# Kernel tuning notes

Measured on AMD Instinct MI355X. Metric: run time of the kernel, lower is better.

The kernel has to match this reference:

```python
import jax, jax.numpy as jnp
import numpy as np

EMB = 1024
E = 8        # num_experts
TOPK = 2
HID = 2048   # expert_dim

def setup_inputs() -> dict:
    key = jax.random.key(0)
    ks = jax.random.split(key, 10)
    s = lambda fan_in: 1.0 / np.sqrt(fan_in)
    x  = jax.random.normal(ks[0], (2, 2048, EMB), dtype=jnp.float32)
    Wr = jax.random.normal(ks[1], (EMB, E), dtype=jnp.float32) * s(EMB)
    br = jnp.zeros((E,), dtype=jnp.float32)
    # stacked expert weights, stored (in, out) so y = x @ W + b
    W1 = jax.random.normal(ks[2], (E, EMB, HID), dtype=jnp.float32) * s(EMB)
    b1 = jax.random.normal(ks[3], (E, HID), dtype=jnp.float32) * 0.01
    Wg = jax.random.normal(ks[4], (E, HID, HID), dtype=jnp.float32) * s(HID)
    bg = jax.random.normal(ks[5], (E, HID), dtype=jnp.float32) * 0.01
    W2 = jax.random.normal(ks[6], (E, HID, EMB), dtype=jnp.float32) * s(HID)
    b2 = jax.random.normal(ks[7], (E, EMB), dtype=jnp.float32) * 0.01
    return {"x": x, "Wr": Wr, "br": br, "W1": W1, "b1": b1,
            "Wg": Wg, "bg": bg, "W2": W2, "b2": b2}

def reference(x, Wr, br, W1, b1, Wg, bg, W2, b2):
    B, S, D = x.shape
    xt = x.reshape(B * S, D)                                  # [T, D]
    logits = xt @ Wr + br                                     # [T, E]
    probs = jax.nn.softmax(logits, axis=-1)
    topk_p, topk_i = jax.lax.top_k(probs, TOPK)               # [T, K]
    # dense gate matrix (top-k probs, NOT renormalized, as in source)
    gates = jnp.sum(jax.nn.one_hot(topk_i, E, dtype=xt.dtype) * topk_p[..., None], axis=1)  # [T, E]
    # expert MLP: layer1 (no act) -> relu(linear) -> layer2, for all experts
    h = jnp.einsum('td,edh->teh', xt, W1) + b1                # [T, E, HID]
    h = jax.nn.relu(jnp.einsum('teh,ehg->teg', h, Wg) + bg)   # [T, E, HID]
    y = jnp.einsum('teh,ehd->ted', h, W2) + b2                # [T, E, D]
    out = jnp.einsum('te,ted->td', gates, y)                  # weighted combine
    return out.reshape(B, S, D)
```

## Files before the change

### kernel.cpp

```cpp
#include <hip/hip_runtime.h>
#include <hip/hip_bf16.h>
#include <stdint.h>

#define NTOK 4096
#define EMBD 1024
#define NEXP 8
#define HIDD 2048
#define NPAIR (NTOK * 2)

typedef __attribute__((ext_vector_type(8))) __bf16 bf16x8;
typedef __attribute__((ext_vector_type(4))) float f32x4;

union V16 { uint4 u; bf16x8 b; };

__device__ __forceinline__ uint16_t f2bf(float f) {
    uint32_t u = __float_as_uint(f);
    return (uint16_t)((u + 0x7FFFu + ((u >> 16) & 1u)) >> 16);
}
__device__ __forceinline__ float bf2f(uint16_t u) {
    return __uint_as_float(((uint32_t)u) << 16);
}
__device__ __forceinline__ void gl_lds16(const uint16_t* g, uint16_t* l) {
    __builtin_amdgcn_global_load_lds(
        (const __attribute__((address_space(1))) void*)g,
        (__attribute__((address_space(3))) void*)l, 16, 0, 0);
}

#define W1_TILES 4096
#define WG_TILES 8192
#define W2_TILES 4096
__global__ __launch_bounds__(256) void transcast3_kernel(
    const float* __restrict__ W1, const float* __restrict__ Wg,
    const float* __restrict__ W2, uint16_t* __restrict__ W1t,
    uint16_t* __restrict__ Wgt, uint16_t* __restrict__ W2t) {
    int id = blockIdx.x;
    const float* src; uint16_t* dst; int K, N;
    if (id < W1_TILES) { src = W1; dst = W1t; K = EMBD; N = HIDD; }
    else if (id < W1_TILES + WG_TILES) { id -= W1_TILES; src = Wg; dst = Wgt; K = HIDD; N = HIDD; }
    else { id -= W1_TILES + WG_TILES; src = W2; dst = W2t; K = HIDD; N = EMBD; }
    int tn = N >> 6, tk = K >> 6;
    int per_e = tn * tk;
    int e = id / per_e, r = id % per_e;
    int n0 = (r % tn) * 64, k0 = (r / tn) * 64;

    __shared__ uint16_t tile[64][68];
    const float* S = src + ((size_t)e * K + k0) * N + n0;
    uint16_t* D = dst + ((size_t)e * N + n0) * K + k0;
    int t = threadIdx.x;
    int rn = (t & 15) * 4, rk = t >> 4;
#pragma unroll
    for (int p = 0; p < 4; p++) {
        int k = rk + p * 16;
        float4 v = *(const float4*)(S + (size_t)k * N + rn);
        ushort4 o;
        o.x = f2bf(v.x); o.y = f2bf(v.y); o.z = f2bf(v.z); o.w = f2bf(v.w);
        *(ushort4*)&tile[k][rn] = o;
    }
    __syncthreads();
    int wn = t >> 3, wk = (t & 7) * 8;
#pragma unroll
    for (int p = 0; p < 2; p++) {
        int n = wn + p * 32;
        uint32_t w0 = (uint32_t)tile[wk + 0][n] | ((uint32_t)tile[wk + 1][n] << 16);
        uint32_t w1 = (uint32_t)tile[wk + 2][n] | ((uint32_t)tile[wk + 3][n] << 16);
        uint32_t w2 = (uint32_t)tile[wk + 4][n] | ((uint32_t)tile[wk + 5][n] << 16);
        uint32_t w3 = (uint32_t)tile[wk + 6][n] | ((uint32_t)tile[wk + 7][n] << 16);
        uint4 pk = {w0, w1, w2, w3};
        *(uint4*)(D + (size_t)n * K + wk) = pk;
    }
}

__global__ __launch_bounds__(64) void router_kernel(const float* __restrict__ x,
                                                    const float* __restrict__ Wr,
                                                    const float* __restrict__ br,
                                                    uint16_t* __restrict__ xb,
                                                    int* __restrict__ counts,
                                                    int* __restrict__ pair_e,
                                                    float* __restrict__ pair_p) {
    int tok = blockIdx.x;
    int lane = threadIdx.x;
    const float* xr = x + (size_t)tok * EMBD;
    uint16_t* xbr = xb + (size_t)tok * EMBD;
    float acc[NEXP];
#pragma unroll
    for (int e = 0; e < NEXP; e++) acc[e] = 0.f;
    for (int d = lane; d < EMBD; d += 64) {
        float xv = xr[d];
        xbr[d] = f2bf(xv);
#pragma unroll
        for (int e = 0; e < NEXP; e++) acc[e] += xv * Wr[d * NEXP + e];
    }
#pragma unroll
    for (int e = 0; e < NEXP; e++) {
#pragma unroll
        for (int off = 32; off > 0; off >>= 1)
            acc[e] += __shfl_down(acc[e], off, 64);
    }
    if (lane == 0) {
        float lg[NEXP];
#pragma unroll
        for (int e = 0; e < NEXP; e++) lg[e] = acc[e] + br[e];
        int e0 = 0;
#pragma unroll
        for (int e = 1; e < NEXP; e++) if (lg[e] > lg[e0]) e0 = e;
        int e1 = (e0 == 0) ? 1 : 0;
#pragma unroll
        for (int e = 0; e < NEXP; e++) if (e != e0 && lg[e] > lg[e1]) e1 = e;
        float mx = lg[0];
#pragma unroll
        for (int e = 1; e < NEXP; e++) mx = fmaxf(mx, lg[e]);
        float s = 0.f, p[NEXP];
#pragma unroll
        for (int e = 0; e < NEXP; e++) { p[e] = __expf(lg[e] - mx); s += p[e]; }
        float inv = 1.f / s;
        pair_e[tok * 2 + 0] = e0; pair_p[tok * 2 + 0] = p[e0] * inv;
        pair_e[tok * 2 + 1] = e1; pair_p[tok * 2 + 1] = p[e1] * inv;
        atomicAdd(&counts[e0], 1);
        atomicAdd(&counts[e1], 1);
    }
}

__global__ __launch_bounds__(256) void scatter_kernel(const int* __restrict__ pair_e,
                                                      const int* __restrict__ counts,
                                                      int* __restrict__ cursors,
                                                      int* __restrict__ toklist,
                                                      int* __restrict__ posmap) {
    int i = blockIdx.x * 256 + threadIdx.x;
    int e = pair_e[i];
    int offs = 0;
    for (int j = 0; j < NEXP; j++) offs += (j < e) ? counts[j] : 0;
    int pos = offs + atomicAdd(&cursors[e], 1);
    toklist[pos] = i >> 1;
    posmap[i] = pos;
}

template <int KDIM, int NDIM, bool GATHER_A, bool RELU>
__global__ __launch_bounds__(256) void gemm_kernel(
    const uint16_t* __restrict__ Abase, const uint16_t* __restrict__ Btbase,
    const float* __restrict__ bbase, uint16_t* __restrict__ Out,
    const int* __restrict__ counts, const int* __restrict__ toklist) {
    int e = blockIdx.z;
    int offs = 0;
    for (int j = 0; j < NEXP; j++) offs += (j < e) ? counts[j] : 0;
    int n_e = counts[e];
    int m0 = blockIdx.y * 128;
    if (m0 >= n_e) return;
    int n0 = blockIdx.x * 128;
    const uint16_t* Bt = Btbase + (size_t)e * NDIM * KDIM;

    __shared__ uint16_t As[128 * 32];
    __shared__ uint16_t Bs[128 * 32];

    int tid = threadIdx.x;
    int lane = tid & 63;
    int wave = tid >> 6;

    int sr = tid >> 2;
    int ss = tid & 3;
    const uint16_t* arp[2];
    const uint16_t* brp[2];
#pragma unroll
    for (int p = 0; p < 2; p++) {
        int r = p * 64 + sr;
        int gs = ss ^ ((r >> 1) & 3);
        int grow;
        if (GATHER_A) {
            int idx = m0 + r;
            if (idx >= n_e) idx = 0;
            grow = toklist[offs + idx];
        } else {
            grow = offs + m0 + r;
        }
        arp[p] = Abase + (size_t)grow * KDIM + gs * 8;
        brp[p] = Bt + (size_t)(n0 + r) * KDIM + gs * 8;
    }
    uint16_t* alds[2] = { &As[wave * 512], &As[2048 + wave * 512] };
    uint16_t* blds[2] = { &Bs[wave * 512], &Bs[2048 + wave * 512] };

    int wm = (wave >> 1) * 64;
    int wn = (wave & 1) * 64;
    int l16 = lane & 15, qd = lane >> 4;
    const uint16_t* afp[4];
    const uint16_t* bfp[4];
#pragma unroll
    for (int t = 0; t < 4; t++) {
        int ar = wm + t * 16 + l16;
        afp[t] = &As[ar * 32 + (qd ^ ((ar >> 1) & 3)) * 8];
        int br = wn + t * 16 + l16;
        bfp[t] = &Bs[br * 32 + (qd ^ ((br >> 1) & 3)) * 8];
    }

    f32x4 acc[4][4];
    f32x4 zero = {0.f, 0.f, 0.f, 0.f};
#pragma unroll
    for (int i = 0; i < 4; i++)
#pragma unroll
        for (int j = 0; j < 4; j++) acc[i][j] = zero;

    for (int kb = 0; kb < KDIM; kb += 32) {
#pragma unroll
        for (int p = 0; p < 2; p++) {
            gl_lds16(arp[p] + kb, alds[p]);
            gl_lds16(brp[p] + kb, blds[p]);
        }
        __syncthreads();
        V16 af[4], bf[4];
#pragma unroll
        for (int t = 0; t < 4; t++) {
            af[t].u = *(const uint4*)(afp[t]);
            bf[t].u = *(const uint4*)(bfp[t]);
        }
#pragma unroll
        for (int i = 0; i < 4; i++)
#pragma unroll
            for (int j = 0; j < 4; j++)
                acc[i][j] = __builtin_amdgcn_mfma_f32_16x16x32_bf16(
                    af[i].b, bf[j].b, acc[i][j], 0, 0, 0);
        __syncthreads();
    }

    const float* bias = bbase + (size_t)e * NDIM;
    int mrem = n_e - m0;
#pragma unroll
    for (int i = 0; i < 4; i++) {
        int rb = wm + i * 16 + qd * 4;
#pragma unroll
        for (int j = 0; j < 4; j++) {
            int col = n0 + wn + j * 16 + l16;
            float bv = bias[col];
#pragma unroll
            for (int r = 0; r < 4; r++) {
                int lr = rb + r;
                if (lr < mrem) {
                    float v = acc[i][j][r] + bv;
                    if (RELU) v = fmaxf(v, 0.f);
                    Out[(size_t)(offs + m0 + lr) * NDIM + col] = f2bf(v);
                }
            }
        }
    }
}

__global__ __launch_bounds__(256) void combine_kernel(const uint16_t* __restrict__ y,
                                                      const int* __restrict__ posmap,
                                                      const float* __restrict__ pair_p,
                                                      float* __restrict__ out) {
    int t = blockIdx.x;
    int d4 = threadIdx.x;
    int p0 = posmap[t * 2], p1 = posmap[t * 2 + 1];
    float w0 = pair_p[t * 2], w1 = pair_p[t * 2 + 1];
    ushort4 a = ((const ushort4*)(y + (size_t)p0 * EMBD))[d4];
    ushort4 b = ((const ushort4*)(y + (size_t)p1 * EMBD))[d4];
    float4 o;
    o.x = w0 * bf2f(a.x) + w1 * bf2f(b.x);
    o.y = w0 * bf2f(a.y) + w1 * bf2f(b.y);
    o.z = w0 * bf2f(a.z) + w1 * bf2f(b.z);
    o.w = w0 * bf2f(a.w) + w1 * bf2f(b.w);
    ((float4*)(out + (size_t)t * EMBD))[d4] = o;
}

extern "C" void kernel_launch(void* const* d_in, const int* in_sizes, int n_in,
                              void* d_out, int out_size, void* d_ws, size_t ws_size,
                              hipStream_t stream) {
    const float* x  = (const float*)d_in[0];
    const float* Wr = (const float*)d_in[1];
    const float* br = (const float*)d_in[2];
    const float* W1 = (const float*)d_in[3];
    const float* b1 = (const float*)d_in[4];
    const float* Wg = (const float*)d_in[5];
    const float* bg = (const float*)d_in[6];
    const float* W2 = (const float*)d_in[7];
    const float* b2 = (const float*)d_in[8];
    float* out = (float*)d_out;

    char* ws = (char*)d_ws;
    uint16_t* xb  = (uint16_t*)ws;
    uint16_t* h   = (uint16_t*)(ws + (8ull << 20));
    uint16_t* yb  = h;
    uint16_t* W1t = (uint16_t*)(ws + (40ull << 20));
    uint16_t* g   = W1t;
    uint16_t* Wgt = (uint16_t*)(ws + (72ull << 20));
    uint16_t* W2t = (uint16_t*)(ws + (136ull << 20));
    int* meta = (int*)(ws + (168ull << 20));
    int*   counts  = meta;
    int*   cursors = meta + 8;
    int*   pair_e  = meta + 16;
    int*   toklist = meta + 16 + NPAIR;
    int*   posmap  = meta + 16 + 2 * NPAIR;
    float* pair_p  = (float*)(meta + 16 + 3 * NPAIR);

    hipMemsetAsync(counts, 0, 16 * sizeof(int), stream);

    router_kernel<<<NTOK, 64, 0, stream>>>(x, Wr, br, xb, counts, pair_e, pair_p);
    transcast3_kernel<<<W1_TILES + WG_TILES + W2_TILES, 256, 0, stream>>>(
        W1, Wg, W2, W1t, Wgt, W2t);
    scatter_kernel<<<NPAIR / 256, 256, 0, stream>>>(pair_e, counts, cursors, toklist, posmap);

    gemm_kernel<EMBD, HIDD, true, false>
        <<<dim3(HIDD / 128, NTOK / 128, NEXP), 256, 0, stream>>>(
            xb, W1t, b1, h, counts, toklist);
    gemm_kernel<HIDD, HIDD, false, true>
        <<<dim3(HIDD / 128, NTOK / 128, NEXP), 256, 0, stream>>>(
            h, Wgt, bg, g, counts, toklist);
    gemm_kernel<HIDD, EMBD, false, false>
        <<<dim3(EMBD / 128, NTOK / 128, NEXP), 256, 0, stream>>>(
            g, W2t, b2, yb, counts, toklist);
    combine_kernel<<<NTOK, 256, 0, stream>>>(yb, posmap, pair_p, out);
}
```

Baseline: 735.3 us.

## Double-buffer GEMM with BK=64, compact expert tile grid, fuse router into transcast

The GEMM now uses a K-tile of 64, double-buffered LDS with async global-to-LDS prefetch of the next tile, explicit vmcnt waits, and raw barriers. The 3D grid with early-exit blocks becomes a compact 1D grid over per-expert M-blocks (up to MBMAX = 71), with an XCD-aware block swizzle. launch_bounds is raised to allow two blocks per CU. The router is folded into the weight transpose-cast launch with four tokens per block. Together these aim to overlap loads with MFMA, cut idle blocks and launches, and improve L2 locality, at the cost of more LDS use and fragile hand-written waitcnt logic.

Measured after the change: 689.1 us. -6.3%, faster.

```diff
diff --git a/kernel.cpp b/kernel.cpp
--- a/kernel.cpp
+++ b/kernel.cpp
@@ -7,6 +7,7 @@
 #define NEXP 8
 #define HIDD 2048
 #define NPAIR (NTOK * 2)
+#define MBMAX 71
 
 typedef __attribute__((ext_vector_type(8))) __bf16 bf16x8;
 typedef __attribute__((ext_vector_type(4))) float f32x4;
@@ -26,14 +27,64 @@
         (__attribute__((address_space(3))) void*)l, 16, 0, 0);
 }
 
+#define RT_BLOCKS (NTOK / 4)
 #define W1_TILES 4096
 #define WG_TILES 8192
 #define W2_TILES 4096
-__global__ __launch_bounds__(256) void transcast3_kernel(
+
+__global__ __launch_bounds__(256) void fused_rt_kernel(
+    const float* __restrict__ x, const float* __restrict__ Wr,
+    const float* __restrict__ br, uint16_t* __restrict__ xb,
+    int* __restrict__ counts, int* __restrict__ pair_e, float* __restrict__ pair_p,
     const float* __restrict__ W1, const float* __restrict__ Wg,
     const float* __restrict__ W2, uint16_t* __restrict__ W1t,
     uint16_t* __restrict__ Wgt, uint16_t* __restrict__ W2t) {
-    int id = blockIdx.x;
+    int bid = blockIdx.x;
+    if (bid < RT_BLOCKS) {
+        int tok = bid * 4 + (threadIdx.x >> 6);
+        int lane = threadIdx.x & 63;
+        const float* xr = x + (size_t)tok * EMBD;
+        uint16_t* xbr = xb + (size_t)tok * EMBD;
+        float acc[NEXP];
+#pragma unroll
+        for (int e = 0; e < NEXP; e++) acc[e] = 0.f;
+        for (int d = lane; d < EMBD; d += 64) {
+            float xv = xr[d];
+            xbr[d] = f2bf(xv);
+#pragma unroll
+            for (int e = 0; e < NEXP; e++) acc[e] += xv * Wr[d * NEXP + e];
+        }
+#pragma unroll
+        for (int e = 0; e < NEXP; e++) {
+#pragma unroll
+            for (int off = 32; off > 0; off >>= 1)
+                acc[e] += __shfl_down(acc[e], off, 64);
+        }
+        if (lane == 0) {
+            float lg[NEXP];
+#pragma unroll
+            for (int e = 0; e < NEXP; e++) lg[e] = acc[e] + br[e];
+            int e0 = 0;
+#pragma unroll
+            for (int e = 1; e < NEXP; e++) if (lg[e] > lg[e0]) e0 = e;
+            int e1 = (e0 == 0) ? 1 : 0;
+#pragma unroll
+            for (int e = 0; e < NEXP; e++) if (e != e0 && lg[e] > lg[e1]) e1 = e;
+            float mx = lg[0];
+#pragma unroll
+            for (int e = 1; e < NEXP; e++) mx = fmaxf(mx, lg[e]);
+            float s = 0.f, p[NEXP];
+#pragma unroll
+            for (int e = 0; e < NEXP; e++) { p[e] = __expf(lg[e] - mx); s += p[e]; }
+            float inv = 1.f / s;
+            pair_e[tok * 2 + 0] = e0; pair_p[tok * 2 + 0] = p[e0] * inv;
+            pair_e[tok * 2 + 1] = e1; pair_p[tok * 2 + 1] = p[e1] * inv;
+            atomicAdd(&counts[e0], 1);
+            atomicAdd(&counts[e1], 1);
+        }
+        return;
+    }
+    int id = bid - RT_BLOCKS;
     const float* src; uint16_t* dst; int K, N;
     if (id < W1_TILES) { src = W1; dst = W1t; K = EMBD; N = HIDD; }
     else if (id < W1_TILES + WG_TILES) { id -= W1_TILES; src = Wg; dst = Wgt; K = HIDD; N = HIDD; }
@@ -67,56 +118,6 @@
         uint32_t w3 = (uint32_t)tile[wk + 6][n] | ((uint32_t)tile[wk + 7][n] << 16);
         uint4 pk = {w0, w1, w2, w3};
         *(uint4*)(D + (size_t)n * K + wk) = pk;
-    }
-}
-
-__global__ __launch_bounds__(64) void router_kernel(const float* __restrict__ x,
-                                                    const float* __restrict__ Wr,
-                                                    const float* __restrict__ br,
-                                                    uint16_t* __restrict__ xb,
-                                                    int* __restrict__ counts,
-                                                    int* __restrict__ pair_e,
-                                                    float* __restrict__ pair_p) {
-    int tok = blockIdx.x;
-    int lane = threadIdx.x;
-    const float* xr = x + (size_t)tok * EMBD;
-    uint16_t* xbr = xb + (size_t)tok * EMBD;
-    float acc[NEXP];
-#pragma unroll
-    for (int e = 0; e < NEXP; e++) acc[e] = 0.f;
-    for (int d = lane; d < EMBD; d += 64) {
-        float xv = xr[d];
-        xbr[d] = f2bf(xv);
-#pragma unroll
-        for (int e = 0; e < NEXP; e++) acc[e] += xv * Wr[d * NEXP + e];
-    }
-#pragma unroll
-    for (int e = 0; e < NEXP; e++) {
-#pragma unroll
-        for (int off = 32; off > 0; off >>= 1)
-            acc[e] += __shfl_down(acc[e], off, 64);
-    }
-    if (lane == 0) {
-        float lg[NEXP];
-#pragma unroll
-        for (int e = 0; e < NEXP; e++) lg[e] = acc[e] + br[e];
-        int e0 = 0;
-#pragma unroll
-        for (int e = 1; e < NEXP; e++) if (lg[e] > lg[e0]) e0 = e;
-        int e1 = (e0 == 0) ? 1 : 0;
-#pragma unroll
-        for (int e = 0; e < NEXP; e++) if (e != e0 && lg[e] > lg[e1]) e1 = e;
-        float mx = lg[0];
-#pragma unroll
-        for (int e = 1; e < NEXP; e++) mx = fmaxf(mx, lg[e]);
-        float s = 0.f, p[NEXP];
-#pragma unroll
-        for (int e = 0; e < NEXP; e++) { p[e] = __expf(lg[e] - mx); s += p[e]; }
-        float inv = 1.f / s;
-        pair_e[tok * 2 + 0] = e0; pair_p[tok * 2 + 0] = p[e0] * inv;
-        pair_e[tok * 2 + 1] = e1; pair_p[tok * 2 + 1] = p[e1] * inv;
-        atomicAdd(&counts[e0], 1);
-        atomicAdd(&counts[e1], 1);
     }
 }
 
@@ -134,35 +135,48 @@
     posmap[i] = pos;
 }
 
-template <int KDIM, int NDIM, bool GATHER_A, bool RELU>
-__global__ __launch_bounds__(256) void gemm_kernel(
+template <int KDIM, int NDIM, int NXB, bool GATHER_A, bool RELU>
+__global__ __launch_bounds__(256, 2) void gemm_kernel(
     const uint16_t* __restrict__ Abase, const uint16_t* __restrict__ Btbase,
     const float* __restrict__ bbase, uint16_t* __restrict__ Out,
     const int* __restrict__ counts, const int* __restrict__ toklist) {
-    int e = blockIdx.z;
-    int offs = 0;
-    for (int j = 0; j < NEXP; j++) offs += (j < e) ? counts[j] : 0;
-    int n_e = counts[e];
-    int m0 = blockIdx.y * 128;
-    if (m0 >= n_e) return;
-    int n0 = blockIdx.x * 128;
+    constexpr int NWG = NXB * MBMAX;
+    constexpr int CPX = NWG / 8;
+    int bid = blockIdx.x;
+    int swz = (bid & 7) * CPX + (bid >> 3);
+    int f = swz / NXB;
+    int nx = swz % NXB;
+
+    int e = NEXP, mloc = 0, offs = 0, n_e = 0;
+    {
+        int acc = 0, o = 0;
+#pragma unroll
+        for (int j = 0; j < NEXP; j++) {
+            int c = counts[j];
+            int mb = (c + 127) >> 7;
+            if (e == NEXP && f < acc + mb) { e = j; mloc = f - acc; offs = o; n_e = c; }
+            acc += mb; o += c;
+        }
+    }
+    if (e == NEXP) return;
+    int m0 = mloc * 128;
+    int n0 = nx * 128;
     const uint16_t* Bt = Btbase + (size_t)e * NDIM * KDIM;
 
-    __shared__ uint16_t As[128 * 32];
-    __shared__ uint16_t Bs[128 * 32];
+    __shared__ __align__(16) uint16_t As[2][128 * 64];
+    __shared__ __align__(16) uint16_t Bs[2][128 * 64];
 
     int tid = threadIdx.x;
     int lane = tid & 63;
     int wave = tid >> 6;
 
-    int sr = tid >> 2;
-    int ss = tid & 3;
-    const uint16_t* arp[2];
-    const uint16_t* brp[2];
-#pragma unroll
-    for (int p = 0; p < 2; p++) {
-        int r = p * 64 + sr;
-        int gs = ss ^ ((r >> 1) & 3);
+    const uint16_t* asrc[4];
+    const uint16_t* bsrc[4];
+#pragma unroll
+    for (int i = 0; i < 4; i++) {
+        int a16 = i * 256 + tid;
+        int r = a16 >> 3, s = a16 & 7;
+        int g = s ^ (r & 7);
         int grow;
         if (GATHER_A) {
             int idx = m0 + r;
@@ -171,23 +185,23 @@
         } else {
             grow = offs + m0 + r;
         }
-        arp[p] = Abase + (size_t)grow * KDIM + gs * 8;
-        brp[p] = Bt + (size_t)(n0 + r) * KDIM + gs * 8;
-    }
-    uint16_t* alds[2] = { &As[wave * 512], &As[2048 + wave * 512] };
-    uint16_t* blds[2] = { &Bs[wave * 512], &Bs[2048 + wave * 512] };
+        asrc[i] = Abase + (size_t)grow * KDIM + g * 8;
+        bsrc[i] = Bt + (size_t)(n0 + r) * KDIM + g * 8;
+    }
 
     int wm = (wave >> 1) * 64;
     int wn = (wave & 1) * 64;
     int l16 = lane & 15, qd = lane >> 4;
-    const uint16_t* afp[4];
-    const uint16_t* bfp[4];
+    int o_a[4][2], o_b[4][2];
 #pragma unroll
     for (int t = 0; t < 4; t++) {
         int ar = wm + t * 16 + l16;
-        afp[t] = &As[ar * 32 + (qd ^ ((ar >> 1) & 3)) * 8];
         int br = wn + t * 16 + l16;
-        bfp[t] = &Bs[br * 32 + (qd ^ ((br >> 1) & 3)) * 8];
+#pragma unroll
+        for (int ks = 0; ks < 2; ks++) {
+            o_a[t][ks] = ar * 64 + (((ks << 2) | qd) ^ (ar & 7)) * 8;
+            o_b[t][ks] = br * 64 + (((ks << 2) | qd) ^ (br & 7)) * 8;
+        }
     }
 
     f32x4 acc[4][4];
@@ -197,26 +211,45 @@
 #pragma unroll
         for (int j = 0; j < 4; j++) acc[i][j] = zero;
 
-    for (int kb = 0; kb < KDIM; kb += 32) {
-#pragma unroll
-        for (int p = 0; p < 2; p++) {
-            gl_lds16(arp[p] + kb, alds[p]);
-            gl_lds16(brp[p] + kb, blds[p]);
-        }
-        __syncthreads();
-        V16 af[4], bf[4];
-#pragma unroll
-        for (int t = 0; t < 4; t++) {
-            af[t].u = *(const uint4*)(afp[t]);
-            bf[t].u = *(const uint4*)(bfp[t]);
-        }
-#pragma unroll
-        for (int i = 0; i < 4; i++)
-#pragma unroll
-            for (int j = 0; j < 4; j++)
-                acc[i][j] = __builtin_amdgcn_mfma_f32_16x16x32_bf16(
-                    af[i].b, bf[j].b, acc[i][j], 0, 0, 0);
-        __syncthreads();
+    constexpr int NK = KDIM / 64;
+#pragma unroll
+    for (int i = 0; i < 4; i++) {
+        gl_lds16(asrc[i], &As[0][i * 2048 + wave * 512]);
+        gl_lds16(bsrc[i], &Bs[0][i * 2048 + wave * 512]);
+    }
+
+    for (int kb = 0; kb < NK; kb++) {
+        int cur = kb & 1;
+        int nxt = cur ^ 1;
+        if (kb + 1 < NK) {
+#pragma unroll
+            for (int i = 0; i < 4; i++) {
+                gl_lds16(asrc[i] + (kb + 1) * 64, &As[nxt][i * 2048 + wave * 512]);
+                gl_lds16(bsrc[i] + (kb + 1) * 64, &Bs[nxt][i * 2048 + wave * 512]);
+            }
+            asm volatile("s_waitcnt vmcnt(8)" ::: "memory");
+        } else {
+            asm volatile("s_waitcnt vmcnt(0)" ::: "memory");
+        }
+        __builtin_amdgcn_s_barrier();
+
+        V16 af[4][2], bf[4][2];
+#pragma unroll
+        for (int t = 0; t < 4; t++)
+#pragma unroll
+            for (int ks = 0; ks < 2; ks++) {
+                af[t][ks].u = *(const uint4*)(&As[cur][o_a[t][ks]]);
+                bf[t][ks].u = *(const uint4*)(&Bs[cur][o_b[t][ks]]);
+            }
+#pragma unroll
+        for (int t = 0; t < 4; t++)
+#pragma unroll
+            for (int u = 0; u < 4; u++)
+#pragma unroll
+                for (int ks = 0; ks < 2; ks++)
+                    acc[t][u] = __builtin_amdgcn_mfma_f32_16x16x32_bf16(
+                        af[t][ks].b, bf[u][ks].b, acc[t][u], 0, 0, 0);
+        __builtin_amdgcn_s_barrier();
     }
 
     const float* bias = bbase + (size_t)e * NDIM;
@@ -291,19 +324,15 @@
 
     hipMemsetAsync(counts, 0, 16 * sizeof(int), stream);
 
-    router_kernel<<<NTOK, 64, 0, stream>>>(x, Wr, br, xb, counts, pair_e, pair_p);
-    transcast3_kernel<<<W1_TILES + WG_TILES + W2_TILES, 256, 0, stream>>>(
-        W1, Wg, W2, W1t, Wgt, W2t);
+    fused_rt_kernel<<<RT_BLOCKS + W1_TILES + WG_TILES + W2_TILES, 256, 0, stream>>>(
+        x, Wr, br, xb, counts, pair_e, pair_p, W1, Wg, W2, W1t, Wgt, W2t);
     scatter_kernel<<<NPAIR / 256, 256, 0, stream>>>(pair_e, counts, cursors, toklist, posmap);
 
-    gemm_kernel<EMBD, HIDD, true, false>
-        <<<dim3(HIDD / 128, NTOK / 128, NEXP), 256, 0, stream>>>(
-            xb, W1t, b1, h, counts, toklist);
-    gemm_kernel<HIDD, HIDD, false, true>
-        <<<dim3(HIDD / 128, NTOK / 128, NEXP), 256, 0, stream>>>(
-            h, Wgt, bg, g, counts, toklist);
-    gemm_kernel<HIDD, EMBD, false, false>
-        <<<dim3(EMBD / 128, NTOK / 128, NEXP), 256, 0, stream>>>(
-            g, W2t, b2, yb, counts, toklist);
+    gemm_kernel<EMBD, HIDD, 16, true, false>
+        <<<16 * MBMAX, 256, 0, stream>>>(xb, W1t, b1, h, counts, toklist);
+    gemm_kernel<HIDD, HIDD, 16, false, true>
+        <<<16 * MBMAX, 256, 0, stream>>>(h, Wgt, bg, g, counts, toklist);
+    gemm_kernel<HIDD, EMBD, 8, false, false>
+        <<<8 * MBMAX, 256, 0, stream>>>(g, W2t, b2, yb, counts, toklist);
     combine_kernel<<<NTOK, 256, 0, stream>>>(yb, posmap, pair_p, out);
 }
```
